# Performance work log

Hardware: AMD Instinct MI355X
Metric: run time of the kernel (lower is better)

Reference implementation:

```python
import jax, jax.numpy as jnp
import numpy as np

N = 100000
E = 1600000
D_IN = 128
D_HID = 128
EDGE_DIM = 1
K_NBR = 16


def _lin_params(key, fan_in, fan_out):
    k1, k2 = jax.random.split(key)
    s = 1.0 / np.sqrt(fan_in)
    W = jax.random.uniform(k1, (fan_in, fan_out), jnp.float32, -s, s)
    b = jax.random.uniform(k2, (fan_out,), jnp.float32, -s, s)
    return W, b


def setup_inputs() -> dict:
    key = jax.random.key(0)
    ks = jax.random.split(key, 16)
    x = jax.random.normal(ks[0], (N, D_IN), jnp.float32)
    edge_index = jax.random.randint(ks[1], (2, E), 0, N, jnp.int64 if jax.config.jax_enable_x64 else jnp.int32)
    neighbor_indices = jax.random.randint(ks[2], (K_NBR,), 0, N, jnp.int32)
    edge_attr = jax.random.normal(ks[3], (E, EDGE_DIM), jnp.float32)
    # conv1: edge lin (edge_dim -> in), mlp (in -> hid -> hid)
    We1, be1 = _lin_params(ks[4], EDGE_DIM, D_IN)
    W11, b11 = _lin_params(ks[5], D_IN, D_HID)
    W12, b12 = _lin_params(ks[6], D_HID, D_HID)
    # conv2: edge lin (edge_dim -> hid), mlp (hid -> hid -> hid)
    We2, be2 = _lin_params(ks[7], EDGE_DIM, D_HID)
    W21, b21 = _lin_params(ks[8], D_HID, D_HID)
    W22, b22 = _lin_params(ks[9], D_HID, D_HID)
    # policy head
    Wl1, bl1 = _lin_params(ks[10], 3 * D_HID, D_HID)
    Wl2, bl2 = _lin_params(ks[11], D_HID, 1)
    return {
        "x": x, "edge_index": edge_index, "curr_idx": 0, "dest_idx": 99999,
        "neighbor_indices": neighbor_indices, "edge_attr": edge_attr,
        "We1": We1, "be1": be1, "W11": W11, "b11": b11, "W12": W12, "b12": b12,
        "We2": We2, "be2": be2, "W21": W21, "b21": b21, "W22": W22, "b22": b22,
        "Wl1": Wl1, "bl1": bl1, "Wl2": Wl2, "bl2": bl2,
    }


def _gine_conv(x, src, dst, edge_attr, We, be, W1, b1, W2, b2, eps=0.0):
    # PyG GINEConv: message = relu(x_j + lin(edge_attr)), sum-aggregate at target,
    # out = mlp((1+eps)*x + aggr)
    e = edge_attr @ We + be                      # [E, d]
    m = jax.nn.relu(x[src] + e)                  # [E, d] gather + fused add/relu
    aggr = jax.ops.segment_sum(m, dst, num_segments=x.shape[0])  # [N, d]
    h = (1.0 + eps) * x + aggr
    return jax.nn.relu(h @ W1 + b1) @ W2 + b2


def reference(x, edge_index, curr_idx, dest_idx, neighbor_indices, edge_attr,
              We1, be1, W11, b11, W12, b12,
              We2, be2, W21, b21, W22, b22,
              Wl1, bl1, Wl2, bl2):
    src, dst = edge_index[0], edge_index[1]
    # encoder (eval mode: dropout is identity)
    h = _gine_conv(x, src, dst, edge_attr, We1, be1, W11, b11, W12, b12)
    h = jax.nn.relu(h)
    node_embs = _gine_conv(h, src, dst, edge_attr, We2, be2, W21, b21, W22, b22)
    # policy head: batched over neighbors instead of python loop
    curr = node_embs[curr_idx]                   # [d]
    dest = node_embs[dest_idx]                   # [d]
    nbr = node_embs[neighbor_indices]            # [K, d]
    Kn = nbr.shape[0]
    cat = jnp.concatenate(
        [jnp.broadcast_to(curr, (Kn, curr.shape[0])),
         jnp.broadcast_to(dest, (Kn, dest.shape[0])),
         nbr], axis=-1)                          # [K, 3d]
    q = jax.nn.relu(cat @ Wl1 + bl1) @ Wl2 + bl2  # [K, 1]
    return q[:, 0]                               # [K]
```

## Files before the change

kernel.cpp:

```cpp
#include <hip/hip_runtime.h>

constexpr int Nn   = 100000;
constexpr int Ee   = 1600000;
constexpr int D    = 128;
constexpr int NT   = 18;

constexpr int CAPS = 1024;
constexpr int CAP2 = 1024;

constexpr int BMW  = 3136;
constexpr int LOCT = 64;
constexpr int LOCS = 128;
constexpr int MAXM = 96;

#define HDR_CNTS  1
#define HDR_CNTL2 3

constexpr size_t OFF_HDR   = 0;
constexpr size_t OFF_MARKS = 256;
constexpr size_t OFF_BMS   = 400256;
constexpr size_t OFF_A1    = 412800;
constexpr size_t ZERO_BYTES= 937088;
constexpr size_t OFF_SLIST = 937088;
constexpr size_t OFF_L2    = 941184;
constexpr size_t OFF_HS    = 953472;
constexpr size_t OFF_EMB   = 1477760;
constexpr size_t WS_NEED   = 1486976;

__global__ void k_zero(float4* p, int n4) {
    int i = blockIdx.x * blockDim.x + threadIdx.x;
    int stride = gridDim.x * blockDim.x;
    for (; i < n4; i += stride) p[i] = float4{0.f, 0.f, 0.f, 0.f};
}

__device__ __forceinline__ void claim_node(int v, int* markS, int* hdr,
                                           int* Slist, unsigned* bmS) {
    if (atomicCAS(&markS[v], 0, -1) == 0) {
        int s = atomicAdd(&hdr[HDR_CNTS], 1);
        if (s < CAPS) {
            Slist[s] = v;
            atomicOr(&bmS[(unsigned)v >> 5], 1u << (v & 31));
            markS[v] = 2 + s;
        }
    }
}

__global__ void __launch_bounds__(256)
k_scanT(const int* __restrict__ src, const int* __restrict__ dst,
        const int* __restrict__ cur, const int* __restrict__ des,
        const int* __restrict__ nbr,
        int* __restrict__ hdr, int* __restrict__ markS,
        unsigned* __restrict__ bmS, int* __restrict__ Slist,
        int* __restrict__ L2) {
    __shared__ unsigned bm[BMW];
    __shared__ int sT[NT];
    __shared__ int loc[LOCT * 3];
    __shared__ int lcnt, lbase;
    int t = threadIdx.x;
    if (t == 0) lcnt = 0;
    for (int w = t; w < BMW; w += 256) bm[w] = 0u;
    if (t < NT) sT[t] = (t == 0) ? cur[0] : (t == 1) ? des[0] : nbr[t - 2];
    __syncthreads();
    if (t < NT) {
        int v = sT[t];
        atomicOr(&bm[(unsigned)v >> 5], 1u << (v & 31));
        if (blockIdx.x == 0) claim_node(v, markS, hdr, Slist, bmS);
    }
    __syncthreads();
    int stride = gridDim.x * blockDim.x;
    for (int q = blockIdx.x * blockDim.x + t; q < Ee / 4; q += stride) {
        int4 d4 = reinterpret_cast<const int4*>(dst)[q];
        int dsv[4] = {d4.x, d4.y, d4.z, d4.w};
        #pragma unroll
        for (int j = 0; j < 4; ++j) {
            int d = dsv[j];
            if ((bm[(unsigned)d >> 5] >> (d & 31)) & 1u) {
                int slot = 0;
                while (sT[slot] != d) ++slot;
                int e = q * 4 + j;
                int s = src[e];
                claim_node(s, markS, hdr, Slist, bmS);
                int li = atomicAdd(&lcnt, 1);
                if (li < LOCT) {
                    loc[3*li] = s; loc[3*li+1] = e; loc[3*li+2] = slot;
                } else {
                    int idx = atomicAdd(&hdr[HDR_CNTL2], 1);
                    if (idx < CAP2) { L2[3*idx] = s; L2[3*idx+1] = e; L2[3*idx+2] = slot; }
                }
            }
        }
    }
    __syncthreads();
    if (t == 0) {
        int n = lcnt < LOCT ? lcnt : LOCT;
        lcnt = n;
        if (n) lbase = atomicAdd(&hdr[HDR_CNTL2], n);
    }
    __syncthreads();
    for (int i = t; i < lcnt; i += 256) {
        int idx = lbase + i;
        if (idx < CAP2) {
            L2[3*idx] = loc[3*i]; L2[3*idx+1] = loc[3*i+1]; L2[3*idx+2] = loc[3*i+2];
        }
    }
}

__global__ void __launch_bounds__(256)
k_scanSA(const float* __restrict__ x, const int* __restrict__ src,
         const int* __restrict__ dst, const float* __restrict__ ea,
         const float* __restrict__ We1, const float* __restrict__ be1,
         const int* __restrict__ markS, const unsigned* __restrict__ bmS,
         float* __restrict__ A1) {
    __shared__ unsigned bm[BMW];
    __shared__ int loc[LOCS * 3];
    __shared__ int lcnt;
    int t = threadIdx.x;
    if (t == 0) lcnt = 0;
    const uint4* g4 = reinterpret_cast<const uint4*>(bmS);
    for (int w = t; w < BMW / 4; w += 256) reinterpret_cast<uint4*>(bm)[w] = g4[w];
    __syncthreads();
    int stride = gridDim.x * blockDim.x;
    for (int q = blockIdx.x * blockDim.x + t; q < Ee / 4; q += stride) {
        int4 d4 = reinterpret_cast<const int4*>(dst)[q];
        int dsv[4] = {d4.x, d4.y, d4.z, d4.w};
        #pragma unroll
        for (int j = 0; j < 4; ++j) {
            int d = dsv[j];
            if ((bm[(unsigned)d >> 5] >> (d & 31)) & 1u) {
                int v = markS[d];
                if (v >= 2) {
                    int e = q * 4 + j;
                    int li = atomicAdd(&lcnt, 1);
                    if (li < LOCS) {
                        loc[3*li] = src[e]; loc[3*li+1] = e; loc[3*li+2] = v - 2;
                    } else {
                        float a = ea[e];
                        int s = src[e];
                        for (int d0 = 0; d0 < D; ++d0)
                            atomicAdd(&A1[(size_t)(v - 2) * D + d0],
                                      fmaxf(fmaf(a, We1[d0], be1[d0]) + x[(size_t)s * D + d0], 0.f));
                    }
                }
            }
        }
    }
    __syncthreads();
    int n = lcnt < LOCS ? lcnt : LOCS;
    int w = t >> 6, l = t & 63;
    int d0 = l * 2;
    for (int i = w; i < n; i += 4) {
        int s = loc[3*i], e = loc[3*i+1], slot = loc[3*i+2];
        float a = ea[e];
        float2 xv = *reinterpret_cast<const float2*>(&x[(size_t)s * D + d0]);
        float2 wv = *reinterpret_cast<const float2*>(&We1[d0]);
        float2 bv = *reinterpret_cast<const float2*>(&be1[d0]);
        atomicAdd(&A1[(size_t)slot * D + d0],     fmaxf(fmaf(a, wv.x, bv.x) + xv.x, 0.f));
        atomicAdd(&A1[(size_t)slot * D + d0 + 1], fmaxf(fmaf(a, wv.y, bv.y) + xv.y, 0.f));
    }
}

__global__ void k_mlpS(const float* __restrict__ x, const float* __restrict__ A,
                       const int* __restrict__ Slist, const int* __restrict__ hdr,
                       const float* __restrict__ W1, const float* __restrict__ b1,
                       const float* __restrict__ W2, const float* __restrict__ b2,
                       float* __restrict__ Hs) {
    __shared__ float buf[D];
    __shared__ float hid[D];
    int b = blockIdx.x;
    int cnt = hdr[HDR_CNTS];
    if (cnt > CAPS) cnt = CAPS;
    if (b >= cnt) return;
    int t = threadIdx.x;
    int node = Slist[b];
    buf[t] = x[(size_t)node * D + t] + A[(size_t)b * D + t];
    __syncthreads();
    float acc = b1[t];
    #pragma unroll 8
    for (int k = 0; k < D; ++k) acc = fmaf(buf[k], W1[k * D + t], acc);
    hid[t] = fmaxf(acc, 0.f);
    __syncthreads();
    float acc2 = b2[t];
    #pragma unroll 8
    for (int k = 0; k < D; ++k) acc2 = fmaf(hid[k], W2[k * D + t], acc2);
    Hs[(size_t)b * D + t] = fmaxf(acc2, 0.f);
}

__global__ void __launch_bounds__(128)
k_tailT(const float* __restrict__ Hs, const int* __restrict__ L2,
        const int* __restrict__ hdr, const int* __restrict__ markS,
        const int* __restrict__ cur, const int* __restrict__ des,
        const int* __restrict__ nbr, const float* __restrict__ ea,
        const float* __restrict__ We2, const float* __restrict__ be2,
        const float* __restrict__ W21, const float* __restrict__ b21,
        const float* __restrict__ W22, const float* __restrict__ b22,
        float* __restrict__ EMB) {
    __shared__ int sT[NT];
    __shared__ float buf[D];
    __shared__ float hid[D];
    __shared__ int mss[MAXM];
    __shared__ float mea[MAXM];
    __shared__ int mcnt;
    int t = threadIdx.x;
    int b = blockIdx.x;
    if (t == 0) mcnt = 0;
    if (t < NT) sT[t] = (t == 0) ? cur[0] : (t == 1) ? des[0] : nbr[t - 2];
    __syncthreads();
    int node = sT[b];
    for (int j = 0; j < b; ++j) if (sT[j] == node) return;
    int cnt2 = hdr[HDR_CNTL2]; if (cnt2 > CAP2) cnt2 = CAP2;
    for (int i = t; i < cnt2; i += 128) {
        if (L2[3*i + 2] == b) {
            int li = atomicAdd(&mcnt, 1);
            if (li < MAXM) {
                mss[li] = markS[L2[3*i]] - 2;
                mea[li] = ea[L2[3*i + 1]];
            }
        }
    }
    __syncthreads();
    int n = mcnt < MAXM ? mcnt : MAXM;
    float w2 = We2[t], bb2 = be2[t];
    float acc = 0.f;
    for (int i = 0; i < n; ++i) {
        int ss = mss[i];
        if ((unsigned)ss < (unsigned)CAPS)
            acc += fmaxf(fmaf(mea[i], w2, bb2) + Hs[(size_t)ss * D + t], 0.f);
    }
    int sst = markS[node] - 2;
    if ((unsigned)sst >= (unsigned)CAPS) return;
    buf[t] = Hs[(size_t)sst * D + t] + acc;
    __syncthreads();
    float a1 = b21[t];
    #pragma unroll 8
    for (int k = 0; k < D; ++k) a1 = fmaf(buf[k], W21[k * D + t], a1);
    hid[t] = fmaxf(a1, 0.f);
    __syncthreads();
    float a2 = b22[t];
    #pragma unroll 8
    for (int k = 0; k < D; ++k) a2 = fmaf(hid[k], W22[k * D + t], a2);
    EMB[b * D + t] = a2;
}

__global__ void __launch_bounds__(512)
k_policy(const float* __restrict__ EMB,
         const int* __restrict__ cur, const int* __restrict__ des,
         const int* __restrict__ nbr,
         const float* __restrict__ Wl1, const float* __restrict__ bl1,
         const float* __restrict__ Wl2, const float* __restrict__ bl2,
         float* __restrict__ out) {
    __shared__ int sT[NT];
    __shared__ float cat[3 * D];
    __shared__ float part[4][D];
    __shared__ float red[D];
    int tid = threadIdx.x;
    int k = blockIdx.x;
    if (tid < NT) sT[tid] = (tid == 0) ? cur[0] : (tid == 1) ? des[0] : nbr[tid - 2];
    __syncthreads();
    int dsl = (sT[1] == sT[0]) ? 0 : 1;
    int nn = sT[2 + k];
    int nsl = 2 + k;
    for (int j = 0; j < 2 + k; ++j) if (sT[j] == nn) { nsl = j; break; }
    if (tid < 3 * D) {
        int seg = tid >> 7;
        int t = tid & (D - 1);
        int slot = (seg == 0) ? 0 : (seg == 1) ? dsl : nsl;
        cat[tid] = EMB[slot * D + t];
    }
    __syncthreads();
    int h = tid >> 7;
    int t = tid & (D - 1);
    float acc = 0.f;
    int c0 = h * 96;
    #pragma unroll 8
    for (int c = c0; c < c0 + 96; ++c)
        acc = fmaf(cat[c], Wl1[c * D + t], acc);
    part[h][t] = acc;
    __syncthreads();
    if (tid < D) {
        float v = part[0][t] + part[1][t] + part[2][t] + part[3][t] + bl1[t];
        red[t] = fmaxf(v, 0.f) * Wl2[t];
    }
    __syncthreads();
    for (int s = 64; s > 0; s >>= 1) {
        if (tid < s) red[tid] += red[tid + s];
        __syncthreads();
    }
    if (tid == 0) out[k] = red[0] + bl2[0];
}

extern "C" void kernel_launch(void* const* d_in, const int* in_sizes, int n_in,
                              void* d_out, int out_size, void* d_ws, size_t ws_size,
                              hipStream_t stream) {
    if (ws_size < WS_NEED) return;

    const float* x   = (const float*)d_in[0];
    const int*   ei  = (const int*)d_in[1];
    const int*   cur = (const int*)d_in[2];
    const int*   des = (const int*)d_in[3];
    const int*   nbr = (const int*)d_in[4];
    const float* ea  = (const float*)d_in[5];
    const float* We1 = (const float*)d_in[6];
    const float* be1 = (const float*)d_in[7];
    const float* W11 = (const float*)d_in[8];
    const float* b11 = (const float*)d_in[9];
    const float* W12 = (const float*)d_in[10];
    const float* b12 = (const float*)d_in[11];
    const float* We2 = (const float*)d_in[12];
    const float* be2 = (const float*)d_in[13];
    const float* W21 = (const float*)d_in[14];
    const float* b21 = (const float*)d_in[15];
    const float* W22 = (const float*)d_in[16];
    const float* b22 = (const float*)d_in[17];
    const float* Wl1 = (const float*)d_in[18];
    const float* bl1 = (const float*)d_in[19];
    const float* Wl2 = (const float*)d_in[20];
    const float* bl2 = (const float*)d_in[21];
    float* out = (float*)d_out;

    char*     ws    = (char*)d_ws;
    int*      hdr   = (int*)(ws + OFF_HDR);
    int*      markS = (int*)(ws + OFF_MARKS);
    unsigned* bmS   = (unsigned*)(ws + OFF_BMS);
    float*    A1    = (float*)(ws + OFF_A1);
    int*      Slist = (int*)(ws + OFF_SLIST);
    int*      L2    = (int*)(ws + OFF_L2);
    float*    Hs    = (float*)(ws + OFF_HS);
    float*    EMB   = (float*)(ws + OFF_EMB);

    const int* srcp = ei;
    const int* dstp = ei + Ee;

    k_zero  <<<256, 256, 0, stream>>>((float4*)ws, (int)(ZERO_BYTES / 16));
    k_scanT <<<512, 256, 0, stream>>>(srcp, dstp, cur, des, nbr,
                                      hdr, markS, bmS, Slist, L2);
    k_scanSA<<<512, 256, 0, stream>>>(x, srcp, dstp, ea, We1, be1,
                                      markS, bmS, A1);
    k_mlpS  <<<CAPS, 128, 0, stream>>>(x, A1, Slist, hdr, W11, b11, W12, b12, Hs);
    k_tailT <<<NT, 128, 0, stream>>>(Hs, L2, hdr, markS, cur, des, nbr, ea,
                                     We2, be2, W21, b21, W22, b22, EMB);
    k_policy<<<16, 512, 0, stream>>>(EMB, cur, des, nbr, Wl1, bl1, Wl2, bl2, out);
}
```

Before: 56.86 us.

## Drop markS zeroing via bitmap claim, split-K the node MLP kernels

Node claiming now uses an atomicOr on the global bitmap instead of a CAS on markS, so the 400 KB markS array moves out of the zeroed region and no longer has to be cleared each call. A bound check guards stale markS values. k_mlpS becomes a grid-stride kernel with 256 threads that splits each 128-wide dot product across two thread groups, and k_tailT uses 512 threads with a four-way split of both the aggregation and the MLP reductions. The shared bitmap clear is vectorised and the zero kernel's grid is shrunk. Leaving markS uncleared means it relies on stale values being either overwritten or rejected by the bit test and the bound check.

Measured after the change: 47.91 us. 1.19x faster.

```diff
diff --git a/kernel.cpp b/kernel.cpp
--- a/kernel.cpp
+++ b/kernel.cpp
@@ -17,10 +17,10 @@
 #define HDR_CNTL2 3
 
 constexpr size_t OFF_HDR   = 0;
-constexpr size_t OFF_MARKS = 256;
-constexpr size_t OFF_BMS   = 400256;
-constexpr size_t OFF_A1    = 412800;
-constexpr size_t ZERO_BYTES= 937088;
+constexpr size_t OFF_BMS   = 256;
+constexpr size_t OFF_A1    = 12800;
+constexpr size_t ZERO_BYTES= 537088;
+constexpr size_t OFF_MARKS = 537088;
 constexpr size_t OFF_SLIST = 937088;
 constexpr size_t OFF_L2    = 941184;
 constexpr size_t OFF_HS    = 953472;
@@ -35,13 +35,11 @@
 
 __device__ __forceinline__ void claim_node(int v, int* markS, int* hdr,
                                            int* Slist, unsigned* bmS) {
-    if (atomicCAS(&markS[v], 0, -1) == 0) {
+    unsigned bit = 1u << (v & 31);
+    unsigned old = atomicOr(&bmS[(unsigned)v >> 5], bit);
+    if (!(old & bit)) {
         int s = atomicAdd(&hdr[HDR_CNTS], 1);
-        if (s < CAPS) {
-            Slist[s] = v;
-            atomicOr(&bmS[(unsigned)v >> 5], 1u << (v & 31));
-            markS[v] = 2 + s;
-        }
+        if (s < CAPS) { Slist[s] = v; markS[v] = 2 + s; }
     }
 }
 
@@ -58,7 +56,8 @@
     __shared__ int lcnt, lbase;
     int t = threadIdx.x;
     if (t == 0) lcnt = 0;
-    for (int w = t; w < BMW; w += 256) bm[w] = 0u;
+    for (int w = t; w < BMW / 4; w += 256)
+        reinterpret_cast<uint4*>(bm)[w] = uint4{0u, 0u, 0u, 0u};
     if (t < NT) sT[t] = (t == 0) ? cur[0] : (t == 1) ? des[0] : nbr[t - 2];
     __syncthreads();
     if (t < NT) {
@@ -128,7 +127,7 @@
             int d = dsv[j];
             if ((bm[(unsigned)d >> 5] >> (d & 31)) & 1u) {
                 int v = markS[d];
-                if (v >= 2) {
+                if (v >= 2 && (unsigned)(v - 2) < (unsigned)CAPS) {
                     int e = q * 4 + j;
                     int li = atomicAdd(&lcnt, 1);
                     if (li < LOCS) {
@@ -159,33 +158,44 @@
     }
 }
 
-__global__ void k_mlpS(const float* __restrict__ x, const float* __restrict__ A,
-                       const int* __restrict__ Slist, const int* __restrict__ hdr,
-                       const float* __restrict__ W1, const float* __restrict__ b1,
-                       const float* __restrict__ W2, const float* __restrict__ b2,
-                       float* __restrict__ Hs) {
+__global__ void __launch_bounds__(256)
+k_mlpS(const float* __restrict__ x, const float* __restrict__ A,
+       const int* __restrict__ Slist, const int* __restrict__ hdr,
+       const float* __restrict__ W1, const float* __restrict__ b1,
+       const float* __restrict__ W2, const float* __restrict__ b2,
+       float* __restrict__ Hs) {
     __shared__ float buf[D];
     __shared__ float hid[D];
-    int b = blockIdx.x;
+    __shared__ float part[2][D];
     int cnt = hdr[HDR_CNTS];
     if (cnt > CAPS) cnt = CAPS;
-    if (b >= cnt) return;
-    int t = threadIdx.x;
-    int node = Slist[b];
-    buf[t] = x[(size_t)node * D + t] + A[(size_t)b * D + t];
-    __syncthreads();
-    float acc = b1[t];
-    #pragma unroll 8
-    for (int k = 0; k < D; ++k) acc = fmaf(buf[k], W1[k * D + t], acc);
-    hid[t] = fmaxf(acc, 0.f);
-    __syncthreads();
-    float acc2 = b2[t];
-    #pragma unroll 8
-    for (int k = 0; k < D; ++k) acc2 = fmaf(hid[k], W2[k * D + t], acc2);
-    Hs[(size_t)b * D + t] = fmaxf(acc2, 0.f);
-}
-
-__global__ void __launch_bounds__(128)
+    int tid = threadIdx.x;
+    int t = tid & 127, g = tid >> 7;
+    for (int b = blockIdx.x; b < cnt; b += gridDim.x) {
+        if (g == 0) {
+            int node = Slist[b];
+            buf[t] = x[(size_t)node * D + t] + A[(size_t)b * D + t];
+        }
+        __syncthreads();
+        float acc = 0.f;
+        int c0 = g * 64;
+        #pragma unroll 8
+        for (int c = c0; c < c0 + 64; ++c) acc = fmaf(buf[c], W1[c * D + t], acc);
+        part[g][t] = acc;
+        __syncthreads();
+        if (g == 0) hid[t] = fmaxf(part[0][t] + part[1][t] + b1[t], 0.f);
+        __syncthreads();
+        acc = 0.f;
+        #pragma unroll 8
+        for (int c = c0; c < c0 + 64; ++c) acc = fmaf(hid[c], W2[c * D + t], acc);
+        part[g][t] = acc;
+        __syncthreads();
+        if (g == 0) Hs[(size_t)b * D + t] = fmaxf(part[0][t] + part[1][t] + b2[t], 0.f);
+        __syncthreads();
+    }
+}
+
+__global__ void __launch_bounds__(512)
 k_tailT(const float* __restrict__ Hs, const int* __restrict__ L2,
         const int* __restrict__ hdr, const int* __restrict__ markS,
         const int* __restrict__ cur, const int* __restrict__ des,
@@ -197,18 +207,19 @@
     __shared__ int sT[NT];
     __shared__ float buf[D];
     __shared__ float hid[D];
+    __shared__ float part[4][D];
     __shared__ int mss[MAXM];
     __shared__ float mea[MAXM];
     __shared__ int mcnt;
-    int t = threadIdx.x;
+    int tid = threadIdx.x;
     int b = blockIdx.x;
-    if (t == 0) mcnt = 0;
-    if (t < NT) sT[t] = (t == 0) ? cur[0] : (t == 1) ? des[0] : nbr[t - 2];
+    if (tid == 0) mcnt = 0;
+    if (tid < NT) sT[tid] = (tid == 0) ? cur[0] : (tid == 1) ? des[0] : nbr[tid - 2];
     __syncthreads();
     int node = sT[b];
     for (int j = 0; j < b; ++j) if (sT[j] == node) return;
     int cnt2 = hdr[HDR_CNTL2]; if (cnt2 > CAP2) cnt2 = CAP2;
-    for (int i = t; i < cnt2; i += 128) {
+    for (int i = tid; i < cnt2; i += 512) {
         if (L2[3*i + 2] == b) {
             int li = atomicAdd(&mcnt, 1);
             if (li < MAXM) {
@@ -219,26 +230,37 @@
     }
     __syncthreads();
     int n = mcnt < MAXM ? mcnt : MAXM;
+    int t = tid & 127, g = tid >> 7;
     float w2 = We2[t], bb2 = be2[t];
-    float acc = 0.f;
-    for (int i = 0; i < n; ++i) {
+    float a = 0.f;
+    for (int i = g; i < n; i += 4) {
         int ss = mss[i];
         if ((unsigned)ss < (unsigned)CAPS)
-            acc += fmaxf(fmaf(mea[i], w2, bb2) + Hs[(size_t)ss * D + t], 0.f);
-    }
-    int sst = markS[node] - 2;
-    if ((unsigned)sst >= (unsigned)CAPS) return;
-    buf[t] = Hs[(size_t)sst * D + t] + acc;
-    __syncthreads();
-    float a1 = b21[t];
+            a += fmaxf(fmaf(mea[i], w2, bb2) + Hs[(size_t)ss * D + t], 0.f);
+    }
+    part[g][t] = a;
+    __syncthreads();
+    if (g == 0) {
+        int sst = markS[node] - 2;
+        float self = ((unsigned)sst < (unsigned)CAPS) ? Hs[(size_t)sst * D + t] : 0.f;
+        buf[t] = self + part[0][t] + part[1][t] + part[2][t] + part[3][t];
+    }
+    __syncthreads();
+    float acc = 0.f;
+    int c0 = g * 32;
     #pragma unroll 8
-    for (int k = 0; k < D; ++k) a1 = fmaf(buf[k], W21[k * D + t], a1);
-    hid[t] = fmaxf(a1, 0.f);
-    __syncthreads();
-    float a2 = b22[t];
+    for (int c = c0; c < c0 + 32; ++c) acc = fmaf(buf[c], W21[c * D + t], acc);
+    part[g][t] = acc;
+    __syncthreads();
+    if (g == 0) hid[t] = fmaxf(part[0][t] + part[1][t] + part[2][t] + part[3][t] + b21[t], 0.f);
+    __syncthreads();
+    acc = 0.f;
     #pragma unroll 8
-    for (int k = 0; k < D; ++k) a2 = fmaf(hid[k], W22[k * D + t], a2);
-    EMB[b * D + t] = a2;
+    for (int c = c0; c < c0 + 32; ++c) acc = fmaf(hid[c], W22[c * D + t], acc);
+    part[g][t] = acc;
+    __syncthreads();
+    if (g == 0)
+        EMB[b * D + t] = part[0][t] + part[1][t] + part[2][t] + part[3][t] + b22[t];
 }
 
 __global__ void __launch_bounds__(512)
@@ -319,9 +341,9 @@
 
     char*     ws    = (char*)d_ws;
     int*      hdr   = (int*)(ws + OFF_HDR);
-    int*      markS = (int*)(ws + OFF_MARKS);
     unsigned* bmS   = (unsigned*)(ws + OFF_BMS);
     float*    A1    = (float*)(ws + OFF_A1);
+    int*      markS = (int*)(ws + OFF_MARKS);
     int*      Slist = (int*)(ws + OFF_SLIST);
     int*      L2    = (int*)(ws + OFF_L2);
     float*    Hs    = (float*)(ws + OFF_HS);
@@ -330,13 +352,13 @@
     const int* srcp = ei;
     const int* dstp = ei + Ee;
 
-    k_zero  <<<256, 256, 0, stream>>>((float4*)ws, (int)(ZERO_BYTES / 16));
+    k_zero  <<<132, 256, 0, stream>>>((float4*)ws, (int)(ZERO_BYTES / 16));
     k_scanT <<<512, 256, 0, stream>>>(srcp, dstp, cur, des, nbr,
                                       hdr, markS, bmS, Slist, L2);
     k_scanSA<<<512, 256, 0, stream>>>(x, srcp, dstp, ea, We1, be1,
                                       markS, bmS, A1);
-    k_mlpS  <<<CAPS, 128, 0, stream>>>(x, A1, Slist, hdr, W11, b11, W12, b12, Hs);
-    k_tailT <<<NT, 128, 0, stream>>>(Hs, L2, hdr, markS, cur, des, nbr, ea,
+    k_mlpS  <<<320, 256, 0, stream>>>(x, A1, Slist, hdr, W11, b11, W12, b12, Hs);
+    k_tailT <<<NT, 512, 0, stream>>>(Hs, L2, hdr, markS, cur, des, nbr, ea,
                                      We2, be2, W21, b21, W22, b22, EMB);
     k_policy<<<16, 512, 0, stream>>>(EMB, cur, des, nbr, Wl1, bl1, Wl2, bl2, out);
 }
```
